# Optimization experiments

Hardware: AMD Instinct MI355X
Metric: run time of the kernel (lower is better)

The kernel has to match this reference:

```python
import jax, jax.numpy as jnp
import numpy as np

RES = (32, 32, 32)
AABB_MIN = np.array([0.0, 0.0, 0.0], np.float32)
AABB_MAX = np.array([1.0, 1.0, 1.0], np.float32)
POS_DIM = 32          # pos_encode_dim
K = 16                # knn_k
SCALER = jnp.asarray(np.array(RES, np.float32) / (AABB_MAX - AABB_MIN))


def sinusoidal_encoding(x, num_channels, data_range):
    # per-coordinate sin/cos at geometric frequencies -> (..., 3*num_channels)
    freqs = (2.0 ** jnp.arange(num_channels // 2, dtype=jnp.float32)) * jnp.pi / data_range
    xf = x[..., None] * freqs
    enc = jnp.concatenate([jnp.sin(xf), jnp.cos(xf)], axis=-1)  # (..., 3, num_channels)
    return enc.reshape(x.shape[:-1] + (x.shape[-1] * num_channels,))


def make_grid():
    axes = [np.linspace(AABB_MIN[i], AABB_MAX[i], RES[i], dtype=np.float32) for i in range(3)]
    g = np.stack(np.meshgrid(*axes, indexing='ij'), axis=-1).reshape(-1, 3)
    return jnp.asarray(g)  # (M, 3)


def layernorm(x, g, b):
    m = jnp.mean(x, -1, keepdims=True)
    v = jnp.var(x, -1, keepdims=True)
    return (x - m) * jax.lax.rsqrt(v + 1e-5) * g + b


def setup_inputs() -> dict:
    key = jax.random.key(0)
    ks = jax.random.split(key, 8)
    B, N, Cin, Cout = 1, 8192, 32, 64
    Cprov = 3 * POS_DIM  # 96 provided (grid) channels
    vertices = jax.random.uniform(ks[0], (B, N, 3), jnp.float32)
    features = jax.random.normal(ks[1], (B, N, Cin), jnp.float32)
    grid_verts = make_grid()
    grid_feat = sinusoidal_encoding(grid_verts, POS_DIM, float(AABB_MAX[0] - AABB_MIN[0]))
    edge_in = Cin + 3  # neighbor feature + rel_pos (use_rel_pos=True, no encode)

    def lin(k, i, o):
        return jax.random.normal(k, (i, o), jnp.float32) / np.sqrt(i)

    return {
        'vertices': vertices, 'features': features,
        'grid_verts': grid_verts, 'grid_feat': grid_feat,
        'ew1': lin(ks[2], edge_in, Cout), 'eb1': jnp.zeros((Cout,), jnp.float32),
        'eg1': jnp.ones((Cout,), jnp.float32), 'ebt1': jnp.zeros((Cout,), jnp.float32),
        'ew2': lin(ks[3], Cout, Cout), 'eb2': jnp.zeros((Cout,), jnp.float32),
        'ow1': lin(ks[4], Cout + Cprov, Cout), 'ob1': jnp.zeros((Cout,), jnp.float32),
        'og1': jnp.ones((Cout,), jnp.float32), 'obt1': jnp.zeros((Cout,), jnp.float32),
        'ow2': lin(ks[5], Cout, Cout), 'ob2': jnp.zeros((Cout,), jnp.float32),
    }


def reference(vertices, features, grid_verts, grid_feat,
              ew1, eb1, eg1, ebt1, ew2, eb2,
              ow1, ob1, og1, obt1, ow2, ob2):
    B = vertices.shape[0]
    M = grid_verts.shape[0]
    # --- KNN in scaled coordinates (neighbor_search_vertices_scaler) ---
    q = grid_verts * SCALER            # (M,3)
    r = vertices * SCALER              # (B,N,3)
    d2 = (jnp.sum(q * q, -1)[None, :, None]
          + jnp.sum(r * r, -1)[:, None, :]
          - 2.0 * jnp.einsum('md,bnd->bmn', q, r))      # (B,M,N)
    _, idx = jax.lax.top_k(-jax.lax.stop_gradient(d2), K)  # (B,M,K) indices into N
    # --- gather neighbor features and relative positions ---
    nbr_feat = jax.vmap(lambda f, i: f[i])(features, idx)   # (B,M,K,Cin)
    nbr_pos = jax.vmap(lambda v, i: v[i])(vertices, idx)    # (B,M,K,3)
    rel_pos = nbr_pos - grid_verts[None, :, None, :]        # (B,M,K,3)
    e = jnp.concatenate([nbr_feat, rel_pos], axis=-1)
    # --- edge MLP (Linear -> LN -> GELU -> Linear) ---
    h = jax.nn.gelu(layernorm(e @ ew1 + eb1, eg1, ebt1)) @ ew2 + eb2  # (B,M,K,Cout)
    agg = jnp.mean(h, axis=2)                                          # mean reduction
    # --- concat provided grid (sinusoidal) features, out MLP ---
    o = jnp.concatenate(
        [agg, jnp.broadcast_to(grid_feat[None], (B, M, grid_feat.shape[-1]))], axis=-1)
    out = jax.nn.gelu(layernorm(o @ ow1 + ob1, og1, obt1)) @ ow2 + ob2  # (B,M,Cout)
    return out.reshape(B, RES[0], RES[1], RES[2], out.shape[-1])
```

## Files before the change

kernel.cpp:

```cpp
#include <hip/hip_runtime.h>
#include <cfloat>
#include <cstdint>
#include <cmath>

#define NV    8192
#define NM    32768
#define KNN   16
#define CIN   32
#define COUT  64
#define CPROV 96
#define CAPB  8
#define MT    4
#define MLP_BLOCK 1024
#define WPB   (MLP_BLOCK/64)


__device__ __forceinline__ unsigned long long d2key(float d2, unsigned int idx) {
    unsigned int b = __float_as_uint(d2);
    b ^= (b & 0x80000000u) ? 0xFFFFFFFFu : 0x80000000u;
    return ((unsigned long long)b << 32) | idx;
}

__device__ __forceinline__ float key_d2f(unsigned long long key) {
    unsigned int b = (unsigned int)(key >> 32);
    b = (b & 0x80000000u) ? (b ^ 0x80000000u) : ~b;
    return __uint_as_float(b);
}

__device__ __forceinline__ void key_insert(unsigned long long* a,
                                           unsigned long long key) {
#pragma unroll
    for (int i = KNN - 1; i >= 1; --i) {
        unsigned long long hi = (a[i-1] > key) ? a[i-1] : key;
        a[i] = (hi < a[i]) ? hi : a[i];
    }
    a[0] = (key < a[0]) ? key : a[0];
}

__device__ __forceinline__ int bin_of(float x) {
    int b = (int)(x * 32.0f);
    return min(31, max(0, b));
}

__global__ __launch_bounds__(256) void bin_count_kernel(
    const float* __restrict__ verts, int* __restrict__ counts)
{
    int v = blockIdx.x * 256 + threadIdx.x;
    int bx = bin_of(verts[v * 3 + 0]);
    int by = bin_of(verts[v * 3 + 1]);
    int bz = bin_of(verts[v * 3 + 2]);
    atomicAdd(&counts[(bx * 32 + by) * 32 + bz], 1);
}

__global__ __launch_bounds__(1024) void prefix_kernel(
    const int* __restrict__ counts, int* __restrict__ prefix)
{
    __shared__ int lds[1024];
    int tid = threadIdx.x;
    int local[32]; int s = 0;
#pragma unroll
    for (int i = 0; i < 32; ++i) { local[i] = counts[tid * 32 + i]; s += local[i]; }
    lds[tid] = s; __syncthreads();
    for (int off = 1; off < 1024; off <<= 1) {
        int v = (tid >= off) ? lds[tid - off] : 0;
        __syncthreads();
        lds[tid] += v;
        __syncthreads();
    }
    int run = lds[tid] - s;
#pragma unroll
    for (int i = 0; i < 32; ++i) { prefix[tid * 32 + i] = run; run += local[i]; }
    if (tid == 1023) prefix[32768] = run;
}

__global__ __launch_bounds__(256) void radius_kernel(
    const float* __restrict__ grid_verts, const int* __restrict__ prefix,
    float* __restrict__ tau)
{
    int m = blockIdx.x * 256 + threadIdx.x;
    int bx = bin_of(grid_verts[m * 3 + 0]);
    int by = bin_of(grid_verts[m * 3 + 1]);
    int bz = bin_of(grid_verts[m * 3 + 2]);
    int R = 1;
    for (; R < 32; ++R) {
        int cnt = 0;
        int xlo = max(0, bx - R), xhi = min(31, bx + R);
        int ylo = max(0, by - R), yhi = min(31, by + R);
        int zlo = max(0, bz - R), zhi = min(31, bz + R);
        for (int x = xlo; x <= xhi; ++x)
            for (int y = ylo; y <= yhi; ++y) {
                int c = (x * 32 + y) * 32;
                cnt += prefix[c + zhi + 1] - prefix[c + zlo];
            }
        if (cnt >= KNN) break;
    }
    float Rp = (float)(R + 1);
    tau[m] = 3.0f * Rp * Rp;
}

__global__ __launch_bounds__(256) void scatter_kernel(
    const float* __restrict__ verts, const int* __restrict__ prefix,
    int* __restrict__ cursor, float4* __restrict__ vps, int* __restrict__ vidx)
{
    int v = blockIdx.x * 256 + threadIdx.x;
    float x0 = verts[v * 3 + 0], x1 = verts[v * 3 + 1], x2 = verts[v * 3 + 2];
    float r0 = __fmul_rn(x0, 32.0f);
    float r1 = __fmul_rn(x1, 32.0f);
    float r2 = __fmul_rn(x2, 32.0f);
    float rr = __fadd_rn(__fadd_rn(__fmul_rn(r0, r0), __fmul_rn(r1, r1)),
                         __fmul_rn(r2, r2));
    int bx = min(31, max(0, (int)r0));
    int by = min(31, max(0, (int)r1));
    int bz = min(31, max(0, (int)r2));
    int b = (bx * 32 + by) * 32 + bz;
    int pos = prefix[b] + atomicAdd(&cursor[b], 1);
    vps[pos] = make_float4(r0, r1, r2, rr);
    vidx[pos] = v;
}

#define CSWAP(i, j) { unsigned long long x_ = a[i], y_ = a[j]; \
                      bool c_ = x_ < y_; \
                      a[i] = c_ ? x_ : y_; a[j] = c_ ? y_ : x_; }

__global__ __launch_bounds__(1024, 4) void knn_spatial_kernel(
    const float4* __restrict__ vps,
    const int*    __restrict__ vidx,
    const int*    __restrict__ prefix,
    const float*  __restrict__ grid_verts,
    const float*  __restrict__ tau,
    int* __restrict__ knn_idx)
{
    __shared__ unsigned long long buf[8192];
    const int tid  = threadIdx.x;
    const int lane = tid & 63;
    const int w    = tid >> 6;

    const int bx4 = (blockIdx.x >> 6) * 4;
    const int by4 = ((blockIdx.x >> 3) & 7) * 4;
    const int bz4 = (blockIdx.x & 7) * 4;
    const int lx = lane >> 4, ly = (lane >> 2) & 3, lz = lane & 3;
    const int m = ((bx4 + lx) * 32 + (by4 + ly)) * 32 + (bz4 + lz);

    const float q0 = __fmul_rn(grid_verts[m * 3 + 0], 32.0f);
    const float q1 = __fmul_rn(grid_verts[m * 3 + 1], 32.0f);
    const float q2 = __fmul_rn(grid_verts[m * 3 + 2], 32.0f);
    const float qq = __fadd_rn(__fadd_rn(__fmul_rn(q0, q0), __fmul_rn(q1, q1)),
                               __fmul_rn(q2, q2));

    const float tm = tau[m];
    const float bound = tm + 0.13f;
    unsigned int bb = __float_as_uint(bound) ^ 0x80000000u;
    const unsigned long long seed = ((unsigned long long)bb << 32);

    unsigned long long a[KNN];
#pragma unroll
    for (int s = 0; s < KNN; ++s) a[s] = seed;
    float gd = bound;
    int cnt = 0;

    int rs = (int)sqrtf(tm) + 1;
#pragma unroll
    for (int off = 32; off; off >>= 1) rs = max(rs, __shfl_xor(rs, off));

    const int xlo = max(0, bx4 - rs), xhi = min(31, bx4 + 3 + rs);
    const int ylo = max(0, by4 - rs), yhi = min(31, by4 + 3 + rs);
    const int zlo = max(0, bz4 - rs), zhi = min(31, bz4 + 3 + rs);
    const int ny = yhi - ylo + 1;
    const int npair = (xhi - xlo + 1) * ny;

    for (int pi = w; pi < npair; pi += 16) {
        const int x = xlo + pi / ny;
        const int y = ylo + pi % ny;
        const int c = (x * 32 + y) * 32;
        const int pstart = prefix[c + zlo];
        const int pend   = prefix[c + zhi + 1];
        for (int p = pstart; p < pend; ++p) {
            float4 v = vps[p];
            float dot = fmaf(q2, v.z, fmaf(q1, v.y, __fmul_rn(q0, v.x)));
            float d2 = fmaf(-2.0f, dot, __fadd_rn(qq, v.w));
            if (d2 <= gd) {
                unsigned long long key = d2key(d2, (unsigned int)vidx[p]);
                if (cnt < CAPB) { buf[cnt * 1024 + tid] = key; ++cnt; }
                else {
                    key_insert(a, key);
                    gd = key_d2f(a[KNN - 1]);
                }
            }
        }
        int mx = cnt;
#pragma unroll
        for (int off = 32; off; off >>= 1) mx = max(mx, __shfl_xor(mx, off));
        for (int k = 0; k < mx; ++k) {
            unsigned long long key = (k < cnt) ? buf[k * 1024 + tid] : ~0ULL;
            key_insert(a, key);
        }
        if (mx) gd = key_d2f(a[KNN - 1]);
        cnt = 0;
    }

    for (int half = 8; half >= 1; half >>= 1) {
        __syncthreads();
        if (w >= half && w < 2 * half) {
            unsigned long long* dst = &buf[(w - half) * 1024];
#pragma unroll
            for (int s = 0; s < KNN; ++s) dst[s * 64 + lane] = a[s];
        }
        __syncthreads();
        if (w < half) {
            const unsigned long long* src = &buf[w * 1024];
#pragma unroll
            for (int i = 0; i < KNN; ++i) {
                unsigned long long b = src[(KNN - 1 - i) * 64 + lane];
                a[i] = (b < a[i]) ? b : a[i];
            }
            CSWAP(0, 8)  CSWAP(1, 9)  CSWAP(2, 10) CSWAP(3, 11)
            CSWAP(4, 12) CSWAP(5, 13) CSWAP(6, 14) CSWAP(7, 15)
            CSWAP(0, 4)  CSWAP(1, 5)  CSWAP(2, 6)  CSWAP(3, 7)
            CSWAP(8, 12) CSWAP(9, 13) CSWAP(10, 14) CSWAP(11, 15)
            CSWAP(0, 2)  CSWAP(1, 3)  CSWAP(4, 6)  CSWAP(5, 7)
            CSWAP(8, 10) CSWAP(9, 11) CSWAP(12, 14) CSWAP(13, 15)
            CSWAP(0, 1)  CSWAP(2, 3)  CSWAP(4, 5)  CSWAP(6, 7)
            CSWAP(8, 9)  CSWAP(10, 11) CSWAP(12, 13) CSWAP(14, 15)
        }
    }

    if (w == 0) {
#pragma unroll
        for (int s = 0; s < KNN; ++s)
            knn_idx[m * KNN + s] = (int)(a[s] & 0xFFFFFFFFu);
    }
}


__global__ void const_kernel(const float* __restrict__ ew1, float* __restrict__ cst)
{
    int c = threadIdx.x;
    float w0 = ew1[32 * 64 + c], w1 = ew1[33 * 64 + c], w2 = ew1[34 * 64 + c];
    float v[9] = { w0, w1, w2, w0*w0, w1*w1, w2*w2, w0*w1, w0*w2, w1*w2 };
#pragma unroll
    for (int k = 0; k < 9; ++k) {
#pragma unroll
        for (int off = 32; off; off >>= 1) v[k] += __shfl_xor(v[k], off);
    }
    if (c == 0) {
        cst[0] = v[0]; cst[1] = v[1]; cst[2] = v[2];
        cst[3] = v[3]; cst[4] = v[4]; cst[5] = v[5];
        cst[6] = v[6]; cst[7] = v[7]; cst[8] = v[8];
    }
}

__global__ __launch_bounds__(256) void pre_edge_kernel(
    const float* __restrict__ feats, const float* __restrict__ ew1,
    const float* __restrict__ eb1, float* __restrict__ pre,
    float* __restrict__ aux)
{
    int t = blockIdx.x * 256 + threadIdx.x;
    int n = t >> 6, c = t & 63;
    float acc = eb1[c];
#pragma unroll
    for (int i = 0; i < CIN; ++i)
        acc = fmaf(feats[n * CIN + i], ew1[i * COUT + c], acc);
    pre[t] = acc;

    float w0 = ew1[32 * 64 + c], w1 = ew1[33 * 64 + c], w2 = ew1[34 * 64 + c];
    float v[5] = { acc, acc * acc, acc * w0, acc * w1, acc * w2 };
#pragma unroll
    for (int k = 0; k < 5; ++k) {
#pragma unroll
        for (int off = 32; off; off >>= 1) v[k] += __shfl_xor(v[k], off);
    }
    if (c == 0) {
        aux[n * 8 + 0] = v[0]; aux[n * 8 + 1] = v[1];
        aux[n * 8 + 2] = v[2]; aux[n * 8 + 3] = v[3]; aux[n * 8 + 4] = v[4];
    }
}

__device__ __forceinline__ float gelu_fast(float x) {
    float t = fmaf(0.044715f, x * x, 1.0f);
    float u = 0.7978845608028654f * x * t;
    float e = __expf(-2.0f * u);
    return x * __builtin_amdgcn_rcpf(1.0f + e);
}

__device__ __forceinline__ float lane_bcast(float v, int lane) {
    return __uint_as_float(__builtin_amdgcn_readlane(__float_as_uint(v), lane));
}

__global__ __launch_bounds__(MLP_BLOCK) void mlp_kernel(
    const float* __restrict__ verts,
    const float* __restrict__ grid_verts,
    const float* __restrict__ grid_feat,
    const float* __restrict__ pre,
    const float* __restrict__ aux,
    const float* __restrict__ cst,
    const int*   __restrict__ knn_idx,
    const float* __restrict__ ew1,
    const float* __restrict__ eg1, const float* __restrict__ ebt1,
    const float* __restrict__ ew2, const float* __restrict__ eb2,
    const float* __restrict__ ow1, const float* __restrict__ ob1,
    const float* __restrict__ og1, const float* __restrict__ obt1,
    const float* __restrict__ ow2, const float* __restrict__ ob2,
    float* __restrict__ out)
{
    __shared__ float s_ew1r[3 * 64];
    __shared__ float s_ew2[64 * 64];
    __shared__ float s_ow1[160 * 64];
    __shared__ float s_ow2[64 * 64];
    __shared__ float s_eg1[64], s_ebt1[64], s_eb2[64];
    __shared__ float s_ob1[64], s_og1[64], s_obt1[64], s_ob2[64];

    const int tid = threadIdx.x;
    for (int t = tid; t < 3 * 64;  t += MLP_BLOCK) s_ew1r[t] = ew1[32 * 64 + t];
    for (int t = tid; t < 64 * 64; t += MLP_BLOCK) s_ew2[t]  = ew2[t];
    for (int t = tid; t < 160 * 64; t += MLP_BLOCK) s_ow1[t] = ow1[t];
    for (int t = tid; t < 64 * 64; t += MLP_BLOCK) s_ow2[t]  = ow2[t];
    if (tid < 64) {
        s_eg1[tid] = eg1[tid];  s_ebt1[tid] = ebt1[tid]; s_eb2[tid] = eb2[tid];
        s_ob1[tid] = ob1[tid];  s_og1[tid] = og1[tid];
        s_obt1[tid] = obt1[tid]; s_ob2[tid] = ob2[tid];
    }
    __syncthreads();

    const int lane = tid & 63;
    const int wave = tid >> 6;
    const int c    = lane;
    const int grp  = blockIdx.x * WPB + wave;
    const int m0   = __builtin_amdgcn_readfirstlane(grp * MT);

    const float Ws0 = cst[0], Ws1 = cst[1], Ws2 = cst[2];
    const float Gxx = cst[3], Gyy = cst[4], Gzz = cst[5];
    const float Gxy = cst[6], Gxz = cst[7], Gyz = cst[8];

    float gvx[MT], gvy[MT], gvz[MT];
#pragma unroll
    for (int p = 0; p < MT; ++p) {
        gvx[p] = grid_verts[(m0 + p) * 3 + 0];
        gvy[p] = grid_verts[(m0 + p) * 3 + 1];
        gvz[p] = grid_verts[(m0 + p) * 3 + 2];
    }

    float gsum[MT];
#pragma unroll
    for (int p = 0; p < MT; ++p) gsum[p] = 0.0f;

    const float inv64 = 1.0f / 64.0f;
    for (int p = 0; p < MT; ++p) {
        for (int j = 0; j < KNN; ++j) {
            int n = __builtin_amdgcn_readfirstlane(knn_idx[(m0 + p) * KNN + j]);
            float S1  = aux[n * 8 + 0], Q = aux[n * 8 + 1];
            float P1x = aux[n * 8 + 2], P1y = aux[n * 8 + 3], P1z = aux[n * 8 + 4];
            float rx = verts[n * 3 + 0] - gvx[p];
            float ry = verts[n * 3 + 1] - gvy[p];
            float rz = verts[n * 3 + 2] - gvz[p];
            float hv = pre[(size_t)n * COUT + c];
            hv = fmaf(rx, s_ew1r[0 * 64 + c], hv);
            hv = fmaf(ry, s_ew1r[1 * 64 + c], hv);
            hv = fmaf(rz, s_ew1r[2 * 64 + c], hv);
            float s1 = S1 + rx * Ws0 + ry * Ws1 + rz * Ws2;
            float s2 = Q + 2.0f * (rx * P1x + ry * P1y + rz * P1z)
                     + rx * rx * Gxx + ry * ry * Gyy + rz * rz * Gzz
                     + 2.0f * (rx * ry * Gxy + rx * rz * Gxz + ry * rz * Gyz);
            float mean = s1 * inv64;
            float var  = s2 * inv64 - mean * mean;
            float xn = (hv - mean) * rsqrtf(var + 1e-5f);
            gsum[p] += gelu_fast(xn * s_eg1[c] + s_ebt1[c]);
        }
    }

    float A[MT];
#pragma unroll
    for (int p = 0; p < MT; ++p) { gsum[p] *= (1.0f / 16.0f); A[p] = s_eb2[c]; }
    for (int jj = 0; jj < 64; ++jj) {
        float w = s_ew2[jj * 64 + c];
#pragma unroll
        for (int p = 0; p < MT; ++p)
            A[p] = fmaf(lane_bcast(gsum[p], jj), w, A[p]);
    }

    float gfa[MT], gfb[MT];
#pragma unroll
    for (int p = 0; p < MT; ++p) {
        gfa[p] = grid_feat[(size_t)(m0 + p) * CPROV + c];
        gfb[p] = grid_feat[(size_t)(m0 + p) * CPROV + 64 + (c & 31)];
    }
    float t1[MT];
#pragma unroll
    for (int p = 0; p < MT; ++p) t1[p] = s_ob1[c];
    for (int jj = 0; jj < 64; ++jj) {
        float w = s_ow1[jj * 64 + c];
#pragma unroll
        for (int p = 0; p < MT; ++p)
            t1[p] = fmaf(lane_bcast(A[p], jj), w, t1[p]);
    }
    for (int i = 0; i < 64; ++i) {
        float w = s_ow1[(64 + i) * 64 + c];
#pragma unroll
        for (int p = 0; p < MT; ++p)
            t1[p] = fmaf(lane_bcast(gfa[p], i), w, t1[p]);
    }
    for (int i = 0; i < 32; ++i) {
        float w = s_ow1[(128 + i) * 64 + c];
#pragma unroll
        for (int p = 0; p < MT; ++p)
            t1[p] = fmaf(lane_bcast(gfb[p], i), w, t1[p]);
    }

#pragma unroll
    for (int p = 0; p < MT; ++p) {
        float x = t1[p];
        float s = x, s2 = x * x;
#pragma unroll
        for (int off = 32; off; off >>= 1) {
            s  += __shfl_xor(s, off);
            s2 += __shfl_xor(s2, off);
        }
        float mean = s * inv64;
        float var  = s2 * inv64 - mean * mean;
        float xn = (x - mean) * rsqrtf(var + 1e-5f);
        t1[p] = gelu_fast(xn * s_og1[c] + s_obt1[c]);
    }

    float o[MT];
#pragma unroll
    for (int p = 0; p < MT; ++p) o[p] = s_ob2[c];
    for (int jj = 0; jj < 64; ++jj) {
        float w = s_ow2[jj * 64 + c];
#pragma unroll
        for (int p = 0; p < MT; ++p)
            o[p] = fmaf(lane_bcast(t1[p], jj), w, o[p]);
    }
#pragma unroll
    for (int p = 0; p < MT; ++p)
        out[(size_t)(m0 + p) * COUT + c] = o[p];
}

extern "C" void kernel_launch(void* const* d_in, const int* in_sizes, int n_in,
                              void* d_out, int out_size, void* d_ws, size_t ws_size,
                              hipStream_t stream)
{
    const float* verts  = (const float*)d_in[0];
    const float* feats  = (const float*)d_in[1];
    const float* gverts = (const float*)d_in[2];
    const float* gfeat  = (const float*)d_in[3];
    const float* ew1    = (const float*)d_in[4];
    const float* eb1    = (const float*)d_in[5];
    const float* eg1    = (const float*)d_in[6];
    const float* ebt1   = (const float*)d_in[7];
    const float* ew2    = (const float*)d_in[8];
    const float* eb2    = (const float*)d_in[9];
    const float* ow1    = (const float*)d_in[10];
    const float* ob1    = (const float*)d_in[11];
    const float* og1    = (const float*)d_in[12];
    const float* obt1   = (const float*)d_in[13];
    const float* ow2    = (const float*)d_in[14];
    const float* ob2    = (const float*)d_in[15];
    float* out = (float*)d_out;

    char* ws = (char*)d_ws;
    int*    counts  = (int*)(ws + 0);
    int*    cursor  = (int*)(ws + 131072);
    int*    prefix  = (int*)(ws + 262144);
    float*  tau     = (float*)(ws + 393224);
    int*    knn_idx = (int*)(ws + 524296);
    float4* vps     = (float4*)(ws + 2621456);
    int*    vidx    = (int*)(ws + 2752528);
    float*  pre     = (float*)(ws + 2785296);
    float*  aux     = (float*)(ws + 4882448);
    float*  cst     = (float*)(ws + 5144592);

    hipMemsetAsync(counts, 0, 262144, stream);
    bin_count_kernel<<<NV / 256, 256, 0, stream>>>(verts, counts);
    prefix_kernel<<<1, 1024, 0, stream>>>(counts, prefix);
    radius_kernel<<<NM / 256, 256, 0, stream>>>(gverts, prefix, tau);
    scatter_kernel<<<NV / 256, 256, 0, stream>>>(verts, prefix, cursor, vps, vidx);
    knn_spatial_kernel<<<NM / 64, 1024, 0, stream>>>(vps, vidx, prefix, gverts, tau, knn_idx);
    pre_edge_kernel<<<(NV * COUT) / 256, 256, 0, stream>>>(feats, ew1, eb1, pre, aux);
    const_kernel<<<1, 64, 0, stream>>>(ew1, cst);
    mlp_kernel<<<NM / (MT * WPB), MLP_BLOCK, 0, stream>>>(verts, gverts, gfeat,
        pre, aux, cst, knn_idx,
        ew1, eg1, ebt1, ew2, eb2, ow1, ob1, og1, obt1, ow2, ob2, out);
}
```

Baseline: 308.4 us.

## Prune KNN cell columns by distance bound and distribute edge LN stats across lanes

The KNN search now uses the wave-wide max of tau to set the search radius. It then skips (x,y) cell columns whose minimum distance already exceeds the bound, and narrows the z range per column to a sphere-derived extent. This cuts the number of candidate points scanned. In the MLP kernel, each of the 64 lanes computes the layernorm statistics for one (point, neighbor) pair, and the results are broadcast across lanes instead of every lane redundantly computing them, with the loops fully unrolled. The costs are extra index arithmetic, clamping, and more lane broadcasts.

Measured after the change: 286.4 us. -7.1%, faster.

```diff
diff --git a/kernel.cpp b/kernel.cpp
--- a/kernel.cpp
+++ b/kernel.cpp
@@ -158,44 +158,61 @@
     float gd = bound;
     int cnt = 0;
 
-    int rs = (int)sqrtf(tm) + 1;
-#pragma unroll
-    for (int off = 32; off; off >>= 1) rs = max(rs, __shfl_xor(rs, off));
-
+    float tmax = tm;
+#pragma unroll
+    for (int off = 32; off; off >>= 1)
+        tmax = fmaxf(tmax, __uint_as_float(__shfl_xor(__float_as_uint(tmax), off)));
+
+    int rs = (int)sqrtf(tmax) + 1;
+    rs = min(31, max(1, rs));
     const int xlo = max(0, bx4 - rs), xhi = min(31, bx4 + 3 + rs);
     const int ylo = max(0, by4 - rs), yhi = min(31, by4 + 3 + rs);
-    const int zlo = max(0, bz4 - rs), zhi = min(31, bz4 + 3 + rs);
     const int ny = yhi - ylo + 1;
     const int npair = (xhi - xlo + 1) * ny;
 
+    int xx = xlo + w / ny;
+    int yy = ylo + w % ny;
     for (int pi = w; pi < npair; pi += 16) {
-        const int x = xlo + pi / ny;
-        const int y = ylo + pi % ny;
-        const int c = (x * 32 + y) * 32;
-        const int pstart = prefix[c + zlo];
-        const int pend   = prefix[c + zhi + 1];
-        for (int p = pstart; p < pend; ++p) {
-            float4 v = vps[p];
-            float dot = fmaf(q2, v.z, fmaf(q1, v.y, __fmul_rn(q0, v.x)));
-            float d2 = fmaf(-2.0f, dot, __fadd_rn(qq, v.w));
-            if (d2 <= gd) {
-                unsigned long long key = d2key(d2, (unsigned int)vidx[p]);
-                if (cnt < CAPB) { buf[cnt * 1024 + tid] = key; ++cnt; }
-                else {
-                    key_insert(a, key);
-                    gd = key_d2f(a[KNN - 1]);
+        int cdx = max(0, max(bx4 - xx, xx - bx4 - 3));
+        int cdy = max(0, max(by4 - yy, yy - by4 - 3));
+        int mdx = max(0, cdx - 1), mdy = max(0, cdy - 1);
+        float rem = tmax - (float)(mdx * mdx + mdy * mdy);
+        if (rem >= 0.0f) {
+            int zrc = (int)sqrtf(rem) + 1;
+            zrc = min(31, max(0, zrc));
+            const int zl = max(0, bz4 - zrc), zh = min(31, bz4 + 3 + zrc);
+            const int cxx = min(xx, 31);
+            const int c = (cxx * 32 + yy) * 32;
+            int pstart = prefix[c + zl];
+            int pend   = prefix[c + zh + 1];
+            pstart = min(max(pstart, 0), NV);
+            pend   = min(max(pend, pstart), NV);
+            for (int p = pstart; p < pend; ++p) {
+                float4 v = vps[p];
+                float dot = fmaf(q2, v.z, fmaf(q1, v.y, __fmul_rn(q0, v.x)));
+                float d2 = fmaf(-2.0f, dot, __fadd_rn(qq, v.w));
+                if (d2 <= gd) {
+                    unsigned long long key = d2key(d2, (unsigned int)vidx[p]);
+                    if (cnt < CAPB) { buf[cnt * 1024 + tid] = key; ++cnt; }
+                    else {
+                        key_insert(a, key);
+                        gd = key_d2f(a[KNN - 1]);
+                    }
                 }
             }
+            int mx = cnt;
+#pragma unroll
+            for (int off = 32; off; off >>= 1) mx = max(mx, __shfl_xor(mx, off));
+            for (int k = 0; k < mx; ++k) {
+                unsigned long long key = (k < cnt) ? buf[k * 1024 + tid] : ~0ULL;
+                key_insert(a, key);
+            }
+            if (mx) gd = key_d2f(a[KNN - 1]);
+            cnt = 0;
         }
-        int mx = cnt;
-#pragma unroll
-        for (int off = 32; off; off >>= 1) mx = max(mx, __shfl_xor(mx, off));
-        for (int k = 0; k < mx; ++k) {
-            unsigned long long key = (k < cnt) ? buf[k * 1024 + tid] : ~0ULL;
-            key_insert(a, key);
-        }
-        if (mx) gd = key_d2f(a[KNN - 1]);
-        cnt = 0;
+        yy += 16;
+        if (yy > yhi) { yy -= ny; ++xx; }
+        if (yy > yhi) { yy -= ny; ++xx; }
     }
 
     for (int half = 8; half >= 1; half >>= 1) {
@@ -331,38 +348,43 @@
     const float Gxx = cst[3], Gyy = cst[4], Gzz = cst[5];
     const float Gxy = cst[6], Gxz = cst[7], Gyz = cst[8];
 
-    float gvx[MT], gvy[MT], gvz[MT];
+    const float inv64 = 1.0f / 64.0f;
+
+    const int pp = lane >> 4, jq = lane & 15;
+    const int nl = knn_idx[(m0 + pp) * KNN + jq];
+    float S1  = aux[nl * 8 + 0], Q = aux[nl * 8 + 1];
+    float P1x = aux[nl * 8 + 2], P1y = aux[nl * 8 + 3], P1z = aux[nl * 8 + 4];
+    float rxl = verts[nl * 3 + 0] - grid_verts[(m0 + pp) * 3 + 0];
+    float ryl = verts[nl * 3 + 1] - grid_verts[(m0 + pp) * 3 + 1];
+    float rzl = verts[nl * 3 + 2] - grid_verts[(m0 + pp) * 3 + 2];
+    float s1l = S1 + rxl * Ws0 + ryl * Ws1 + rzl * Ws2;
+    float s2l = Q + 2.0f * (rxl * P1x + ryl * P1y + rzl * P1z)
+              + rxl * rxl * Gxx + ryl * ryl * Gyy + rzl * rzl * Gzz
+              + 2.0f * (rxl * ryl * Gxy + rxl * rzl * Gxz + ryl * rzl * Gyz);
+    float meanl  = s1l * inv64;
+    float varl   = s2l * inv64 - meanl * meanl;
+    float irstdl = rsqrtf(varl + 1e-5f);
+
+    float gsum[MT];
+#pragma unroll
+    for (int p = 0; p < MT; ++p) gsum[p] = 0.0f;
+
 #pragma unroll
     for (int p = 0; p < MT; ++p) {
-        gvx[p] = grid_verts[(m0 + p) * 3 + 0];
-        gvy[p] = grid_verts[(m0 + p) * 3 + 1];
-        gvz[p] = grid_verts[(m0 + p) * 3 + 2];
-    }
-
-    float gsum[MT];
-#pragma unroll
-    for (int p = 0; p < MT; ++p) gsum[p] = 0.0f;
-
-    const float inv64 = 1.0f / 64.0f;
-    for (int p = 0; p < MT; ++p) {
+#pragma unroll
         for (int j = 0; j < KNN; ++j) {
+            const int src = p * 16 + j;
             int n = __builtin_amdgcn_readfirstlane(knn_idx[(m0 + p) * KNN + j]);
-            float S1  = aux[n * 8 + 0], Q = aux[n * 8 + 1];
-            float P1x = aux[n * 8 + 2], P1y = aux[n * 8 + 3], P1z = aux[n * 8 + 4];
-            float rx = verts[n * 3 + 0] - gvx[p];
-            float ry = verts[n * 3 + 1] - gvy[p];
-            float rz = verts[n * 3 + 2] - gvz[p];
             float hv = pre[(size_t)n * COUT + c];
+            float rx = lane_bcast(rxl, src);
+            float ry = lane_bcast(ryl, src);
+            float rz = lane_bcast(rzl, src);
             hv = fmaf(rx, s_ew1r[0 * 64 + c], hv);
             hv = fmaf(ry, s_ew1r[1 * 64 + c], hv);
             hv = fmaf(rz, s_ew1r[2 * 64 + c], hv);
-            float s1 = S1 + rx * Ws0 + ry * Ws1 + rz * Ws2;
-            float s2 = Q + 2.0f * (rx * P1x + ry * P1y + rz * P1z)
-                     + rx * rx * Gxx + ry * ry * Gyy + rz * rz * Gzz
-                     + 2.0f * (rx * ry * Gxy + rx * rz * Gxz + ry * rz * Gyz);
-            float mean = s1 * inv64;
-            float var  = s2 * inv64 - mean * mean;
-            float xn = (hv - mean) * rsqrtf(var + 1e-5f);
+            float mean  = lane_bcast(meanl, src);
+            float irstd = lane_bcast(irstdl, src);
+            float xn = (hv - mean) * irstd;
             gsum[p] += gelu_fast(xn * s_eg1[c] + s_ebt1[c]);
         }
     }
```
